# Optimization experiments

Hardware: AMD Instinct MI355X
Metric: run time of the kernel (lower is better)

The kernel has to match this reference:

```python
import jax, jax.numpy as jnp
import numpy as np

N = 200000       # active voxels
C_IN = 64
C_OUT = 64
K = 3            # kernel size -> 27 offsets
BS = 2
SHAPE = (256, 256, 256)


def setup_inputs() -> dict:
    # unique active voxel coordinates (b, x, y, z)
    rng = np.random.default_rng(0)
    vol = SHAPE[0] * SHAPE[1] * SHAPE[2]
    lin = rng.choice(BS * vol, size=N, replace=False).astype(np.int64)
    b = lin // vol
    r = lin % vol
    x = r // (SHAPE[1] * SHAPE[2])
    r = r % (SHAPE[1] * SHAPE[2])
    y = r // SHAPE[2]
    z = r % SHAPE[2]
    coords = jnp.asarray(np.stack([b, x, y, z], axis=1).astype(np.int32))

    key = jax.random.key(0)
    k1, k2 = jax.random.split(key)
    features = jax.random.normal(k1, (N, C_IN), dtype=jnp.float32)
    # xavier_uniform over the full [K,K,K,C_in,C_out] kernel (bias init to 0, per module)
    fan_in, fan_out = 27 * C_IN, 27 * C_OUT
    limit = float(np.sqrt(6.0 / (fan_in + fan_out)))
    weight = jax.random.uniform(k2, (27, C_IN, C_OUT), dtype=jnp.float32,
                                minval=-limit, maxval=limit)
    bias = jnp.zeros((C_OUT,), dtype=jnp.float32)
    return {
        "features": features,
        "coords": coords,
        "weight": weight,
        "bias": bias,
        "spatial_shape": jnp.asarray(SHAPE, dtype=jnp.int32),
        "bs": BS,
    }


def _build_rulebook(coords, spatial_shape):
    """For every active site and each of the 27 offsets, find the index of the
    active neighbor at coord+offset, or n (invalid) if absent. Returns [27, n]."""
    n = coords.shape[0]
    X, Y, Z = spatial_shape[0], spatial_shape[1], spatial_shape[2]
    b, x, y, z = coords[:, 0], coords[:, 1], coords[:, 2], coords[:, 3]
    keys = ((b * X + x) * Y + y) * Z + z                      # [n] unique linear keys
    order = jnp.argsort(keys)
    skeys = keys[order]

    d = jnp.arange(-(K // 2), K // 2 + 1, dtype=jnp.int32)
    ox, oy, oz = jnp.meshgrid(d, d, d, indexing="ij")
    offs = jnp.stack([ox.ravel(), oy.ravel(), oz.ravel()], axis=1)  # [27,3]

    nxyz = coords[None, :, 1:4] + offs[:, None, :]            # [27,n,3]
    lim = jnp.stack([X, Y, Z]).astype(jnp.int32)
    inb = jnp.all((nxyz >= 0) & (nxyz < lim[None, None, :]), axis=-1)  # [27,n]
    qk = ((b[None, :] * X + nxyz[..., 0]) * Y + nxyz[..., 1]) * Z + nxyz[..., 2]

    pos = jnp.searchsorted(skeys, qk)                         # [27,n]
    posc = jnp.clip(pos, 0, n - 1)
    found = inb & (pos < n) & (skeys[posc] == qk)
    return jnp.where(found, order[posc], n)                   # n == padded zero row


def reference(features, coords, weight, bias, spatial_shape, bs):
    n = features.shape[0]
    idx = _build_rulebook(coords, spatial_shape)              # [27,n]
    feats_pad = jnp.concatenate(
        [features, jnp.zeros((1, features.shape[1]), features.dtype)], axis=0)

    def step(acc, xk):
        idx_k, w_k = xk
        # gather-GEMM-scatter for one kernel offset (submanifold: out sites = in sites)
        return acc + feats_pad[idx_k] @ w_k, None

    init = jnp.broadcast_to(bias.astype(features.dtype), (n, weight.shape[2]))
    out, _ = jax.lax.scan(step, init, (idx, weight))
    return out
```

## Files before the change

kernel.cpp:

```cpp
#include <hip/hip_runtime.h>
#include <cstdint>
#include <cstddef>


typedef __attribute__((ext_vector_type(8))) short bf16x8;
typedef __attribute__((ext_vector_type(4))) float f32x4;

static constexpr unsigned long long EMPTY64 = ~0ull;
static constexpr int LCAP = 512;
static constexpr unsigned NREGION = 27;
static constexpr unsigned CPAD = 16;
static constexpr int PB = 48;
static constexpr int NBWORDS = 1 << 20;

__device__ __forceinline__ unsigned hash_mix(unsigned key) {
    unsigned h = key * 0x9E3779B1u;
    h ^= h >> 15;
    return h;
}

__device__ __forceinline__ unsigned short f2bf(float x) {
    unsigned u = __builtin_bit_cast(unsigned, x);
    return (unsigned short)((u + 0x7FFFu + ((u >> 16) & 1u)) >> 16);
}

__global__ void init_table_kernel(unsigned long long* __restrict__ table,
                                  int nslots, unsigned* __restrict__ bitmap,
                                  int nbwords, unsigned* __restrict__ cnts,
                                  const float* __restrict__ weight,
                                  unsigned short* __restrict__ wfrag) {
    int i = blockIdx.x * blockDim.x + threadIdx.x;
    if (i < nslots) table[i] = EMPTY64;
    if (i < nbwords) bitmap[i] = 0u;
    if (i < 512) {
        cnts[i] = 0u;
        const int lane = i & 63, nt = (i >> 6) & 3, ks = i >> 8;
        const float* __restrict__ w13 = weight + 13 * 4096;
        #pragma unroll
        for (int j = 0; j < 8; ++j) {
            const int k = ks * 32 + (lane >> 4) * 8 + j;
            const int n = nt * 16 + (lane & 15);
            wfrag[(size_t)i * 8 + j] = f2bf(w13[k * 64 + n]);
        }
    }
}

__global__ void insert_kernel(const int4* __restrict__ coords, int n,
                              unsigned long long* __restrict__ table,
                              unsigned mask, unsigned* __restrict__ bitmap) {
    int i = blockIdx.x * blockDim.x + threadIdx.x;
    if (i >= n) return;
    const int4 c = coords[i];
    const unsigned key = ((unsigned)c.x << 24) | ((unsigned)c.y << 16) |
                         ((unsigned)c.z << 8) | (unsigned)c.w;
    const unsigned w = ((((unsigned)c.x << 8) | (unsigned)c.y) << 11) |
                       (((unsigned)c.z >> 2) << 5) | ((unsigned)c.w >> 3);
    const unsigned bit = (((unsigned)c.z & 3u) << 3) | ((unsigned)c.w & 7u);
    atomicOr(&bitmap[w], 1u << bit);
    const unsigned long long entry =
        (unsigned long long)key | ((unsigned long long)(unsigned)i << 32);
    unsigned s = hash_mix(key) & mask;
    while (atomicCAS((unsigned long long*)&table[s], EMPTY64, entry) !=
           EMPTY64)
        s = (s + 1) & mask;
}

__global__ __launch_bounds__(512) void probe_pairs_kernel(
    const int4* __restrict__ coords, int n,
    const unsigned long long* __restrict__ table, unsigned mask,
    const unsigned* __restrict__ bitmap,
    unsigned* __restrict__ cnts, uint2* __restrict__ pairs, unsigned rcap)
{
    __shared__ unsigned lcnt;
    __shared__ unsigned lk[32], lkb[32], lkp[32];
    __shared__ uint2 lbuf[LCAP];
    if (threadIdx.x == 0) lcnt = 0u;
    if (threadIdx.x < 32) lk[threadIdx.x] = 0u;
    __syncthreads();

    const int site = blockIdx.x * blockDim.x + threadIdx.x;
    if (site < n) {
        const int4 c = coords[site];
        const int b = c.x, x = c.y, y = c.z, z = c.w;
        const int r = y & 3, yt = y >> 2;
        const int s = z & 7, zt = z >> 3;
        const bool redge = (r == 0) || (r == 3);
        const int yta = (r == 0) ? yt - 1 : yt + 1;
        const bool vya = (r == 0) ? (y > 0) : (y < 255);
        const bool zl = (s == 0) && (z > 0);
        const bool zh = (s == 7) && (z < 255);
        const bool vxm = (x > 0);
        const int xm = x - 1;

        #define BWORD(xx, ytt, ztt) \
            bitmap[((((unsigned)b << 8) | (unsigned)(xx)) << 11) | \
                   ((unsigned)(ytt) << 5) | (unsigned)(ztt)]

        const unsigned Pm  = vxm ? BWORD(xm, yt, zt) : 0u;
        const unsigned Pa  = (vxm && redge && vya) ? BWORD(xm, yta, zt) : 0u;
        const unsigned Pml = (vxm && zl) ? BWORD(xm, yt, zt - 1) : 0u;
        const unsigned Pal = (vxm && redge && vya && zl)
                                 ? BWORD(xm, yta, zt - 1) : 0u;
        const unsigned Pmh = (vxm && zh) ? BWORD(xm, yt, zt + 1) : 0u;
        const unsigned Pah = (vxm && redge && vya && zh)
                                 ? BWORD(xm, yta, zt + 1) : 0u;
        const unsigned Qm  = BWORD(x, yt, zt);
        const bool qa = (r == 0) && (y > 0);
        const unsigned Qa  = qa ? BWORD(x, yt - 1, zt) : 0u;
        const unsigned Qml = zl ? BWORD(x, yt, zt - 1) : 0u;
        const unsigned Qal = (qa && zl) ? BWORD(x, yt - 1, zt - 1) : 0u;
        const unsigned Qmh = zh ? BWORD(x, yt, zt + 1) : 0u;
        const unsigned Qah = (qa && zh) ? BWORD(x, yt - 1, zt + 1) : 0u;
        #undef BWORD

        const int rm1 = (r == 0) ? 3 : r - 1;
        const int rp1 = (r == 3) ? 0 : r + 1;
        const unsigned PA  = (r == 0) ? Pa : Pm;
        const unsigned PAl = (r == 0) ? Pal : Pml;
        const unsigned PAh = (r == 0) ? Pah : Pmh;
        const unsigned PC  = (r == 3) ? Pa : Pm;
        const unsigned PCl = (r == 3) ? Pal : Pml;
        const unsigned PCh = (r == 3) ? Pah : Pmh;
        const unsigned QA  = (r == 0) ? Qa : Qm;
        const unsigned QAl = (r == 0) ? Qal : Qml;
        const unsigned QAh = (r == 0) ? Qah : Qmh;

        #define ROWB(W, rr) (((W) >> ((rr) * 8)) & 0xFFu)
        unsigned triA, triB, triC, triD, bitE;
        {
            const unsigned cA = ROWB(PA, rm1), cB = ROWB(Pm, r),
                           cC = ROWB(PC, rp1), cD = ROWB(QA, rm1),
                           cE = ROWB(Qm, r);
            if (s == 0) {
                triA = ((cA & 3u) << 1) | (ROWB(PAl, rm1) >> 7);
                triB = ((cB & 3u) << 1) | (ROWB(Pml, r)   >> 7);
                triC = ((cC & 3u) << 1) | (ROWB(PCl, rp1) >> 7);
                triD = ((cD & 3u) << 1) | (ROWB(QAl, rm1) >> 7);
                bitE = ROWB(Qml, r) >> 7;
            } else if (s == 7) {
                triA = ((cA >> 6) & 3u) | ((ROWB(PAh, rm1) & 1u) << 2);
                triB = ((cB >> 6) & 3u) | ((ROWB(Pmh, r)   & 1u) << 2);
                triC = ((cC >> 6) & 3u) | ((ROWB(PCh, rp1) & 1u) << 2);
                triD = ((cD >> 6) & 3u) | ((ROWB(QAh, rm1) & 1u) << 2);
                bitE = (cE >> 6) & 1u;
            } else {
                triA = (cA >> (s - 1)) & 7u;
                triB = (cB >> (s - 1)) & 7u;
                triC = (cC >> (s - 1)) & 7u;
                triD = (cD >> (s - 1)) & 7u;
                bitE = (cE >> (s - 1)) & 1u;
            }
        }
        #undef ROWB
        unsigned hitm = triA | (triB << 3) | (triC << 6) | (triD << 9) |
                        (bitE << 12);

        while (hitm) {
            const int bb = __ffs(hitm) - 1;
            hitm &= hitm - 1;
            const int g = bb / 3, d = bb % 3;
            const int dx = (g < 3) ? -1 : 0;
            const int dy = (g < 3) ? (g - 1) : ((g == 3) ? -1 : 0);
            const int k = 3 * g + d;
            const unsigned key = ((unsigned)b << 24) |
                                 ((unsigned)(x + dx) << 16) |
                                 ((unsigned)(y + dy) << 8) |
                                 (unsigned)(z + d - 1);
            unsigned sl = hash_mix(key) & mask;
            unsigned long long e = table[sl];
            while (e != EMPTY64 && (unsigned)e != key) {
                sl = (sl + 1) & mask;
                e = table[sl];
            }
            if (e == EMPTY64) continue;
            const unsigned nbi = (unsigned)(e >> 32);
            const uint2 p0 = make_uint2((unsigned)site | ((unsigned)k << 18),
                                        nbi);
            const uint2 p1 = make_uint2(nbi | ((unsigned)(26 - k) << 18),
                                        (unsigned)site);
            const unsigned li = atomicAdd(&lcnt, 2u);
            if (li + 1 < (unsigned)LCAP) {
                lbuf[li] = p0;
                lbuf[li + 1] = p1;
            } else {
                const unsigned g0 = atomicAdd(&cnts[k * CPAD], 1u);
                if (g0 < rcap) pairs[(size_t)k * rcap + g0] = p0;
                const unsigned g1 = atomicAdd(&cnts[(26 - k) * CPAD], 1u);
                if (g1 < rcap) pairs[(size_t)(26 - k) * rcap + g1] = p1;
            }
        }
    }

    __syncthreads();
    const unsigned nloc = lcnt < (unsigned)LCAP ? lcnt : (unsigned)LCAP;
    for (unsigned i = threadIdx.x; i < nloc; i += blockDim.x)
        atomicAdd(&lk[lbuf[i].x >> 18], 1u);
    __syncthreads();
    if (threadIdx.x < NREGION) {
        const unsigned c = lk[threadIdx.x];
        lkb[threadIdx.x] = c ? atomicAdd(&cnts[threadIdx.x * CPAD], c) : 0u;
        lkp[threadIdx.x] = 0u;
    }
    __syncthreads();
    for (unsigned i = threadIdx.x; i < nloc; i += blockDim.x) {
        const uint2 e = lbuf[i];
        const unsigned kk = e.x >> 18;
        const unsigned pos = atomicAdd(&lkp[kk], 1u);
        const unsigned idx = lkb[kk] + pos;
        if (idx < rcap) pairs[(size_t)kk * rcap + idx] = e;
    }
}

__global__ __launch_bounds__(256) void conv_center_mfma(
    const float* __restrict__ feats, const unsigned short* __restrict__ wfrag,
    const float* __restrict__ bias, float* __restrict__ out, int n)
{
    const int lane = threadIdx.x & 63;
    const int wid = blockIdx.x * (blockDim.x >> 6) + (threadIdx.x >> 6);
    const int s0 = wid * 16;
    if (s0 >= n) return;

    bf16x8 bfrag[2][4];
    #pragma unroll
    for (int ks = 0; ks < 2; ++ks)
        #pragma unroll
        for (int nt = 0; nt < 4; ++nt)
            bfrag[ks][nt] = *reinterpret_cast<const bf16x8*>(
                wfrag + ((size_t)((ks * 4 + nt) * 64 + lane)) * 8);

    const int arow = s0 + (lane & 15);
    const bool vrow = arow < n;
    const float* __restrict__ fbase =
        feats + (size_t)(vrow ? arow : 0) * 64 + (lane >> 4) * 8;

    f32x4 acc[4] = {{0.f, 0.f, 0.f, 0.f}, {0.f, 0.f, 0.f, 0.f},
                    {0.f, 0.f, 0.f, 0.f}, {0.f, 0.f, 0.f, 0.f}};

    #pragma unroll
    for (int ks = 0; ks < 2; ++ks) {
        const f32x4 flo = *reinterpret_cast<const f32x4*>(fbase + ks * 32);
        const f32x4 fhi = *reinterpret_cast<const f32x4*>(fbase + ks * 32 + 4);
        bf16x8 afrag;
        afrag[0] = (short)f2bf(flo.x); afrag[1] = (short)f2bf(flo.y);
        afrag[2] = (short)f2bf(flo.z); afrag[3] = (short)f2bf(flo.w);
        afrag[4] = (short)f2bf(fhi.x); afrag[5] = (short)f2bf(fhi.y);
        afrag[6] = (short)f2bf(fhi.z); afrag[7] = (short)f2bf(fhi.w);
        #pragma unroll
        for (int nt = 0; nt < 4; ++nt)
            acc[nt] = __builtin_amdgcn_mfma_f32_16x16x32_bf16(
                afrag, bfrag[ks][nt], acc[nt], 0, 0, 0);
    }

    const int crow0 = s0 + (lane >> 4) * 4;
    const int col = lane & 15;
    #pragma unroll
    for (int nt = 0; nt < 4; ++nt) {
        const float bv = bias[nt * 16 + col];
        #pragma unroll
        for (int r = 0; r < 4; ++r) {
            const int sr = crow0 + r;
            if (sr < n)
                out[(size_t)sr * 64 + nt * 16 + col] = acc[nt][r] + bv;
        }
    }
}

__global__ __launch_bounds__(256) void conv_pairs_kernel(
    const float* __restrict__ feats, const float* __restrict__ weight,
    const uint2* __restrict__ pairs, const unsigned* __restrict__ cnts,
    unsigned rcap, float* __restrict__ out)
{
    const int lane = threadIdx.x & 63;
    int r = blockIdx.x / PB;
    r += (r >= 13);
    unsigned cnt = cnts[r * CPAD];
    if (cnt > rcap) cnt = rcap;
    if (cnt == 0) return;
    const uint2* __restrict__ rp = pairs + (size_t)r * rcap;
    const float* __restrict__ wk = weight + (size_t)r * 4096;
    const unsigned wloc = (blockIdx.x % PB) * 4 + (threadIdx.x >> 6);
    for (unsigned p = wloc; p < cnt; p += (unsigned)(PB * 4)) {
        const uint2 pr = rp[p];
        const unsigned site = pr.x & 0x3FFFFu;
        const unsigned nbi = pr.y;
        const float4* __restrict__ fr =
            reinterpret_cast<const float4*>(feats + (size_t)nbi * 64);
        float a0 = 0.f, a1 = 0.f, a2 = 0.f, a3 = 0.f;
        #pragma unroll
        for (int q = 0; q < 16; ++q) {
            const float4 f = fr[q];
            a0 = fmaf(f.x, wk[(4 * q + 0) * 64 + lane], a0);
            a1 = fmaf(f.y, wk[(4 * q + 1) * 64 + lane], a1);
            a2 = fmaf(f.z, wk[(4 * q + 2) * 64 + lane], a2);
            a3 = fmaf(f.w, wk[(4 * q + 3) * 64 + lane], a3);
        }
        atomicAdd(&out[(size_t)site * 64 + lane], (a0 + a1) + (a2 + a3));
    }
}

extern "C" void kernel_launch(void* const* d_in, const int* in_sizes, int n_in,
                              void* d_out, int out_size, void* d_ws, size_t ws_size,
                              hipStream_t stream) {
    const float* feats  = (const float*)d_in[0];
    const int4*  coords = (const int4*)d_in[1];
    const float* weight = (const float*)d_in[2];
    const float* bias   = (const float*)d_in[3];
    float* out = (float*)d_out;

    const int n = in_sizes[1] / 4;

    const bool big = ws_size >= ((size_t)16 << 20);
    const int nslots = big ? (1 << 19) : (1 << 18);
    const unsigned mask = (unsigned)(nslots - 1);
    const int nbclear = NBWORDS + 4;
    unsigned long long* table = (unsigned long long*)d_ws;
    unsigned* bitmap = (unsigned*)(table + nslots);
    unsigned* cnts = bitmap + nbclear;
    unsigned short* wfrag = (unsigned short*)((char*)cnts + 2048);
    uint2* pairs = (uint2*)((char*)wfrag + 8192);
    const size_t used = (size_t)nslots * 8 + (size_t)nbclear * 4 + 2048 + 8192;
    size_t cap_sz = (ws_size > used) ? (ws_size - used) / sizeof(uint2) : 0;
    if (cap_sz > (size_t)(4 << 20)) cap_sz = (size_t)(4 << 20);
    const unsigned rcap = (unsigned)(cap_sz / NREGION);

    {
        const int work = (nslots > nbclear) ? nslots : nbclear;
        int blocks = (work + 255) / 256;
        init_table_kernel<<<blocks, 256, 0, stream>>>(table, nslots, bitmap,
                                                      nbclear, cnts, weight,
                                                      wfrag);
    }
    {
        int blocks = (n + 255) / 256;
        insert_kernel<<<blocks, 256, 0, stream>>>(coords, n, table, mask,
                                                  bitmap);
    }
    {
        int blocks = (n + 511) / 512;
        probe_pairs_kernel<<<blocks, 512, 0, stream>>>(coords, n, table, mask,
                                                       bitmap, cnts, pairs,
                                                       rcap);
    }
    {
        int waves = (n + 15) / 16;
        int blocks = (waves + 3) / 4;
        conv_center_mfma<<<blocks, 256, 0, stream>>>(feats, wfrag, bias, out, n);
    }
    {
        conv_pairs_kernel<<<26 * PB, 256, 0, stream>>>(feats, weight, pairs,
                                                       cnts, rcap, out);
    }
}
```

Measured before the change: 97.76 us.

## Replace hash table with dense voxel index array for neighbor lookup

```diff
diff --git a/kernel.cpp b/kernel.cpp
--- a/kernel.cpp
+++ b/kernel.cpp
@@ -6,31 +6,23 @@
 typedef __attribute__((ext_vector_type(8))) short bf16x8;
 typedef __attribute__((ext_vector_type(4))) float f32x4;
 
-static constexpr unsigned long long EMPTY64 = ~0ull;
 static constexpr int LCAP = 512;
 static constexpr unsigned NREGION = 27;
 static constexpr unsigned CPAD = 16;
 static constexpr int PB = 48;
 static constexpr int NBWORDS = 1 << 20;
-
-__device__ __forceinline__ unsigned hash_mix(unsigned key) {
-    unsigned h = key * 0x9E3779B1u;
-    h ^= h >> 15;
-    return h;
-}
+static constexpr size_t NVOX = (size_t)1 << 25;
 
 __device__ __forceinline__ unsigned short f2bf(float x) {
     unsigned u = __builtin_bit_cast(unsigned, x);
     return (unsigned short)((u + 0x7FFFu + ((u >> 16) & 1u)) >> 16);
 }
 
-__global__ void init_table_kernel(unsigned long long* __restrict__ table,
-                                  int nslots, unsigned* __restrict__ bitmap,
-                                  int nbwords, unsigned* __restrict__ cnts,
-                                  const float* __restrict__ weight,
-                                  unsigned short* __restrict__ wfrag) {
+__global__ void init_kernel(unsigned* __restrict__ bitmap, int nbwords,
+                            unsigned* __restrict__ cnts,
+                            const float* __restrict__ weight,
+                            unsigned short* __restrict__ wfrag) {
     int i = blockIdx.x * blockDim.x + threadIdx.x;
-    if (i < nslots) table[i] = EMPTY64;
     if (i < nbwords) bitmap[i] = 0u;
     if (i < 512) {
         cnts[i] = 0u;
@@ -46,8 +38,8 @@
 }
 
 __global__ void insert_kernel(const int4* __restrict__ coords, int n,
-                              unsigned long long* __restrict__ table,
-                              unsigned mask, unsigned* __restrict__ bitmap) {
+                              unsigned* __restrict__ idx,
+                              unsigned* __restrict__ bitmap) {
     int i = blockIdx.x * blockDim.x + threadIdx.x;
     if (i >= n) return;
     const int4 c = coords[i];
@@ -57,18 +49,12 @@
                        (((unsigned)c.z >> 2) << 5) | ((unsigned)c.w >> 3);
     const unsigned bit = (((unsigned)c.z & 3u) << 3) | ((unsigned)c.w & 7u);
     atomicOr(&bitmap[w], 1u << bit);
-    const unsigned long long entry =
-        (unsigned long long)key | ((unsigned long long)(unsigned)i << 32);
-    unsigned s = hash_mix(key) & mask;
-    while (atomicCAS((unsigned long long*)&table[s], EMPTY64, entry) !=
-           EMPTY64)
-        s = (s + 1) & mask;
+    idx[key] = (unsigned)i;
 }
 
 __global__ __launch_bounds__(512) void probe_pairs_kernel(
     const int4* __restrict__ coords, int n,
-    const unsigned long long* __restrict__ table, unsigned mask,
-    const unsigned* __restrict__ bitmap,
+    const unsigned* __restrict__ idx, const unsigned* __restrict__ bitmap,
     unsigned* __restrict__ cnts, uint2* __restrict__ pairs, unsigned rcap)
 {
     __shared__ unsigned lcnt;
@@ -152,41 +138,43 @@
             }
         }
         #undef ROWB
-        unsigned hitm = triA | (triB << 3) | (triC << 6) | (triD << 9) |
-                        (bitE << 12);
-
-        while (hitm) {
-            const int bb = __ffs(hitm) - 1;
-            hitm &= hitm - 1;
-            const int g = bb / 3, d = bb % 3;
-            const int dx = (g < 3) ? -1 : 0;
-            const int dy = (g < 3) ? (g - 1) : ((g == 3) ? -1 : 0);
-            const int k = 3 * g + d;
-            const unsigned key = ((unsigned)b << 24) |
-                                 ((unsigned)(x + dx) << 16) |
-                                 ((unsigned)(y + dy) << 8) |
-                                 (unsigned)(z + d - 1);
-            unsigned sl = hash_mix(key) & mask;
-            unsigned long long e = table[sl];
-            while (e != EMPTY64 && (unsigned)e != key) {
-                sl = (sl + 1) & mask;
-                e = table[sl];
+        const unsigned hitm = triA | (triB << 3) | (triC << 6) | (triD << 9) |
+                              (bitE << 12);
+
+        if (hitm) {
+            const unsigned skey = ((unsigned)b << 24) | ((unsigned)x << 16) |
+                                  ((unsigned)y << 8) | (unsigned)z;
+            unsigned nbi[13];
+            #pragma unroll
+            for (int bb = 0; bb < 13; ++bb) {
+                if (hitm & (1u << bb)) {
+                    const int g = bb / 3, d = bb % 3;
+                    const int dx = (g < 3) ? -1 : 0;
+                    const int dy = (g < 3) ? (g - 1) : ((g == 3) ? -1 : 0);
+                    const int duv = (dx << 16) + (dy << 8) + (d - 1);
+                    nbi[bb] = idx[(unsigned)((int)skey + duv)];
+                }
             }
-            if (e == EMPTY64) continue;
-            const unsigned nbi = (unsigned)(e >> 32);
-            const uint2 p0 = make_uint2((unsigned)site | ((unsigned)k << 18),
-                                        nbi);
-            const uint2 p1 = make_uint2(nbi | ((unsigned)(26 - k) << 18),
-                                        (unsigned)site);
-            const unsigned li = atomicAdd(&lcnt, 2u);
-            if (li + 1 < (unsigned)LCAP) {
-                lbuf[li] = p0;
-                lbuf[li + 1] = p1;
-            } else {
-                const unsigned g0 = atomicAdd(&cnts[k * CPAD], 1u);
-                if (g0 < rcap) pairs[(size_t)k * rcap + g0] = p0;
-                const unsigned g1 = atomicAdd(&cnts[(26 - k) * CPAD], 1u);
-                if (g1 < rcap) pairs[(size_t)(26 - k) * rcap + g1] = p1;
+            #pragma unroll
+            for (int bb = 0; bb < 13; ++bb) {
+                if (hitm & (1u << bb)) {
+                    const uint2 p0 = make_uint2(
+                        (unsigned)site | ((unsigned)bb << 18), nbi[bb]);
+                    const uint2 p1 = make_uint2(
+                        nbi[bb] | ((unsigned)(26 - bb) << 18), (unsigned)site);
+                    const unsigned li = atomicAdd(&lcnt, 2u);
+                    if (li + 1 < (unsigned)LCAP) {
+                        lbuf[li] = p0;
+                        lbuf[li + 1] = p1;
+                    } else {
+                        const unsigned g0 = atomicAdd(&cnts[bb * CPAD], 1u);
+                        if (g0 < rcap) pairs[(size_t)bb * rcap + g0] = p0;
+                        const unsigned g1 =
+                            atomicAdd(&cnts[(26 - bb) * CPAD], 1u);
+                        if (g1 < rcap)
+                            pairs[(size_t)(26 - bb) * rcap + g1] = p1;
+                    }
+                }
             }
         }
     }
@@ -206,8 +194,8 @@
         const uint2 e = lbuf[i];
         const unsigned kk = e.x >> 18;
         const unsigned pos = atomicAdd(&lkp[kk], 1u);
-        const unsigned idx = lkb[kk] + pos;
-        if (idx < rcap) pairs[(size_t)kk * rcap + idx] = e;
+        const unsigned idxp = lkb[kk] + pos;
+        if (idxp < rcap) pairs[(size_t)kk * rcap + idxp] = e;
     }
 }
 
@@ -309,35 +297,28 @@
 
     const int n = in_sizes[1] / 4;
 
-    const bool big = ws_size >= ((size_t)16 << 20);
-    const int nslots = big ? (1 << 19) : (1 << 18);
-    const unsigned mask = (unsigned)(nslots - 1);
-    const int nbclear = NBWORDS + 4;
-    unsigned long long* table = (unsigned long long*)d_ws;
-    unsigned* bitmap = (unsigned*)(table + nslots);
-    unsigned* cnts = bitmap + nbclear;
+    unsigned* bitmap = (unsigned*)d_ws;
+    unsigned* cnts = bitmap + NBWORDS;
     unsigned short* wfrag = (unsigned short*)((char*)cnts + 2048);
-    uint2* pairs = (uint2*)((char*)wfrag + 8192);
-    const size_t used = (size_t)nslots * 8 + (size_t)nbclear * 4 + 2048 + 8192;
+    unsigned* idxarr = (unsigned*)((char*)wfrag + 8192);
+    uint2* pairs = (uint2*)(idxarr + NVOX);
+    const size_t used = (size_t)NBWORDS * 4 + 2048 + 8192 + NVOX * 4;
     size_t cap_sz = (ws_size > used) ? (ws_size - used) / sizeof(uint2) : 0;
     if (cap_sz > (size_t)(4 << 20)) cap_sz = (size_t)(4 << 20);
     const unsigned rcap = (unsigned)(cap_sz / NREGION);
 
     {
-        const int work = (nslots > nbclear) ? nslots : nbclear;
-        int blocks = (work + 255) / 256;
-        init_table_kernel<<<blocks, 256, 0, stream>>>(table, nslots, bitmap,
-                                                      nbclear, cnts, weight,
-                                                      wfrag);
+        int blocks = (NBWORDS + 255) / 256;
+        init_kernel<<<blocks, 256, 0, stream>>>(bitmap, NBWORDS, cnts,
+                                                weight, wfrag);
     }
     {
         int blocks = (n + 255) / 256;
-        insert_kernel<<<blocks, 256, 0, stream>>>(coords, n, table, mask,
-                                                  bitmap);
+        insert_kernel<<<blocks, 256, 0, stream>>>(coords, n, idxarr, bitmap);
     }
     {
         int blocks = (n + 511) / 512;
-        probe_pairs_kernel<<<blocks, 512, 0, stream>>>(coords, n, table, mask,
+        probe_pairs_kernel<<<blocks, 512, 0, stream>>>(coords, n, idxarr,
                                                        bitmap, cnts, pairs,
                                                        rcap);
     }
```

Result: faster. 81.89 us (-16.2%).
